# Kernel tuning notes

Measured on AMD Instinct MI355X. Metric: run time of the kernel, lower is better.

The kernel has to match this reference:

```python
import jax, jax.numpy as jnp
import numpy as np

# Interpretation constants (external PersistentHomology class unavailable):
# each sample's feature vector is a point cloud of N_POINTS points in R^POINT_DIM.
N_POINTS = 1024
POINT_DIM = 128
WEIGHT = 1.0
N_TARGET_DIMS = 2  # target_dimensions = [0, 1]; H1 diagram is empty -> contributes 0


def _h0_mean_persistence(pts):
    """Exact H0 persistence of the Vietoris-Rips filtration of a point cloud.

    H0 pairs are (birth=0, death=w_e) for each edge w_e of the Euclidean MST,
    so persistence values are exactly the MST edge lengths (Prim's algorithm,
    vectorized over points, sequential over the N-1 tree-growth steps).
    pts: [N, d] -> scalar mean persistence.
    """
    n = pts.shape[0]
    mindist0 = jnp.linalg.norm(pts - pts[0], axis=-1)          # [N]
    visited0 = jnp.zeros((n,), dtype=bool).at[0].set(True)

    def step(carry, _):
        mindist, visited = carry
        masked = jnp.where(visited, jnp.inf, mindist)          # [N]
        j = jnp.argmin(masked)
        death = masked[j]                                      # MST edge length
        visited = visited.at[j].set(True)
        newd = jnp.linalg.norm(pts - pts[j], axis=-1)          # [N]
        mindist = jnp.minimum(mindist, newd)
        return (mindist, visited), death

    (_, _), deaths = jax.lax.scan(step, (mindist0, visited0), None, length=n - 1)
    return jnp.mean(deaths)


def setup_inputs() -> dict:
    key = jax.random.key(0)
    representations = jax.random.normal(key, (128, N_POINTS * POINT_DIM), dtype=jnp.float32)
    return {"representations": representations}


def reference(representations) -> jnp.ndarray:
    b = representations.shape[0]
    pts = representations.reshape(b, N_POINTS, POINT_DIM)      # per-sample point cloud
    per_sample = jax.vmap(_h0_mean_persistence)(pts)           # [B] mean H0 persistence
    # original: sum over batch and target dims (H1 empty), / (B * n_dims), * weight
    loss = jnp.sum(per_sample) / (b * N_TARGET_DIMS)
    return WEIGHT * loss
```

## Files before the change

### kernel.cpp

```cpp
#include <hip/hip_runtime.h>

typedef unsigned int uint_t;
typedef unsigned short ushort_t;
typedef unsigned char uchar_t;
typedef _Float16 h2 __attribute__((ext_vector_type(2)));
typedef _Float16 f16x8 __attribute__((ext_vector_type(8)));
typedef float f32x4 __attribute__((ext_vector_type(4)));

#define NPTS 1024
#define DIM  128
#define NH2  64

__device__ __forceinline__ float dot2f(uint_t a, uint_t b, float c) {
#if __has_builtin(__builtin_amdgcn_fdot2)
    return __builtin_amdgcn_fdot2(__builtin_bit_cast(h2, a),
                                  __builtin_bit_cast(h2, b), c, false);
#else
    h2 ha = __builtin_bit_cast(h2, a);
    h2 hb = __builtin_bit_cast(h2, b);
    c += (float)ha[0] * (float)hb[0];
    c += (float)ha[1] * (float)hb[1];
    return c;
#endif
}

__device__ __forceinline__ uint_t umin_u(uint_t a, uint_t b) { return a < b ? a : b; }
__device__ __forceinline__ uint_t umax_u(uint_t a, uint_t b) { return a > b ? a : b; }
__device__ __forceinline__ uint_t pk_min_u16(uint_t a, uint_t b) {
    uint_t d; asm("v_pk_min_u16 %0, %1, %2" : "=v"(d) : "v"(a), "v"(b)); return d;
}
__device__ __forceinline__ uint_t pk_max_u16(uint_t a, uint_t b) {
    uint_t d; asm("v_pk_max_u16 %0, %1, %2" : "=v"(d) : "v"(a), "v"(b)); return d;
}

#define DPP_UMIN(x, ctrl)                                                       \
    x = umin_u(x, (uint_t)__builtin_amdgcn_update_dpp((int)(x), (int)(x),       \
                                                      (ctrl), 0xf, 0xf, false))
#define DPP_REDUCE(x)                                                           \
    do { DPP_UMIN(x, 0x111); DPP_UMIN(x, 0x112); DPP_UMIN(x, 0x114);            \
         DPP_UMIN(x, 0x118); DPP_UMIN(x, 0x142); DPP_UMIN(x, 0x143); } while (0)

#define SEL_LO 0x05020400u
#define SEL_HI 0x07020600u

__device__ __forceinline__ void gload16(const void* g, void* l) {
#if __has_builtin(__builtin_amdgcn_global_load_lds)
    __builtin_amdgcn_global_load_lds(
        (__attribute__((address_space(1))) void*)(g),
        (__attribute__((address_space(3))) void*)(l), 16, 0, 0);
#else
    *(uint4*)l = *(const uint4*)g;
#endif
}

__global__ __launch_bounds__(256)
void prep_kernel(const float* __restrict__ reps, ushort_t* __restrict__ P16,
                 float* __restrict__ norms) {
    const int t   = threadIdx.x;
    const int row = blockIdx.x * 16 + (t >> 4);
    const int kx  = (t & 15) * 8;
    const float* src = reps + (size_t)row * DIM + kx;
    float4 v0 = *(const float4*)src;
    float4 v1 = *(const float4*)(src + 4);
    _Float16 h[8] = {(_Float16)v0.x, (_Float16)v0.y, (_Float16)v0.z, (_Float16)v0.w,
                     (_Float16)v1.x, (_Float16)v1.y, (_Float16)v1.z, (_Float16)v1.w};
    float nrm = 0.f;
    uint_t pk[4];
#pragma unroll
    for (int i = 0; i < 4; ++i) {
        float a = (float)h[2 * i], b = (float)h[2 * i + 1];
        nrm += a * a + b * b;
        pk[i] = (uint_t)__builtin_bit_cast(ushort_t, h[2 * i]) |
                ((uint_t)__builtin_bit_cast(ushort_t, h[2 * i + 1]) << 16);
    }
    *(uint4*)(P16 + (size_t)row * DIM + kx) = make_uint4(pk[0], pk[1], pk[2], pk[3]);
#pragma unroll
    for (int m = 1; m <= 8; m <<= 1) nrm += __shfl_xor(nrm, m, 16);
    if ((t & 15) == 0) norms[row] = nrm;
}

__global__ __launch_bounds__(256)
void norms_kernel(const float* __restrict__ reps, float* __restrict__ norms) {
    const int t   = threadIdx.x;
    const int row = blockIdx.x * 16 + (t >> 4);
    const int kx  = (t & 15) * 8;
    const float* src = reps + (size_t)row * DIM + kx;
    float4 v0 = *(const float4*)src;
    float4 v1 = *(const float4*)(src + 4);
    float nrm = 0.f;
    {
        _Float16 h[8] = {(_Float16)v0.x, (_Float16)v0.y, (_Float16)v0.z, (_Float16)v0.w,
                         (_Float16)v1.x, (_Float16)v1.y, (_Float16)v1.z, (_Float16)v1.w};
#pragma unroll
        for (int i = 0; i < 8; ++i) { float a = (float)h[i]; nrm += a * a; }
    }
#pragma unroll
    for (int m = 1; m <= 8; m <<= 1) nrm += __shfl_xor(nrm, m, 16);
    if ((t & 15) == 0) norms[row] = nrm;
}

__device__ __forceinline__ int swz(int row, int seg) {
    return (row << 7) + (((seg ^ row) & 15) << 3);
}
__device__ __forceinline__ uint_t packh2(float a, float b) {
    h2 p; p[0] = (_Float16)a; p[1] = (_Float16)b;
    return __builtin_bit_cast(uint_t, p);
}

__device__ __forceinline__ void gram_core_epilogue(
        f32x4 acc[2][8], const float* nrmS, uchar_t* Ds,
        int ti, int tj, int lane, int w) {
    const int cj = lane & 15;
    const int r4 = (lane >> 4) * 4;
    float na[2][4], nb[8];
#pragma unroll
    for (int mt = 0; mt < 2; ++mt)
#pragma unroll
        for (int r = 0; r < 4; ++r)
            na[mt][r] = nrmS[ti * 128 + w * 32 + mt * 16 + r4 + r];
#pragma unroll
    for (int nt = 0; nt < 8; ++nt) nb[nt] = nrmS[tj * 128 + nt * 16 + cj];
#pragma unroll
    for (int mt = 0; mt < 2; ++mt)
#pragma unroll
        for (int nt = 0; nt < 8; ++nt) {
            const int gj = tj * 128 + nt * 16 + cj;
#pragma unroll
            for (int r = 0; r < 4; ++r) {
                const int gi = ti * 128 + w * 32 + mt * 16 + r4 + r;
                float d2 = fmaxf(na[mt][r] + nb[nt] - 2.f * acc[mt][nt][r], 0.f);
                uint_t q = (uint_t)(d2 * 0.5f + 0.5f);
                q = q > 255u ? 255u : q;
                Ds[((size_t)gi << 10) + gj] = (uchar_t)q;
            }
        }
}

__global__ __launch_bounds__(256, 4)
void gram16_kernel(const ushort_t* __restrict__ P16, const float* __restrict__ norms,
                   uchar_t* __restrict__ D8, int xcd_affine) {
    __shared__ ushort_t Bt[128 * 128];
    const int bid = blockIdx.x;
    int s, tile;
    if (xcd_affine) {
        const int x = bid & 7, k = bid >> 3;
        s    = x + ((k >> 6) << 3);
        tile = k & 63;
    } else {
        s    = bid >> 6;
        tile = bid & 63;
    }
    const int ti = tile >> 3, tj = tile & 7;
    const int t  = threadIdx.x, lane = t & 63, w = t >> 6;

    const ushort_t* Pa = P16 + (((size_t)s * NPTS + (size_t)ti * 128) << 7);
    const ushort_t* Pb = P16 + (((size_t)s * NPTS + (size_t)tj * 128) << 7);
#pragma unroll
    for (int i = 0; i < 8; ++i) {
        const int c   = t + i * 256;
        const int row = c >> 4;
        const int seg = (c ^ row) & 15;
        gload16(Pb + ((size_t)row << 7) + (size_t)seg * 8, &Bt[(size_t)c * 8]);
    }

    const int mrow = lane & 15;
    const int lg   = lane >> 4;
    const ushort_t* parow0 = Pa + ((w * 32 + mrow) << 7);
    const ushort_t* parow1 = Pa + ((w * 32 + 16 + mrow) << 7);
    f16x8 a0 = *(const f16x8*)(parow0 + lg * 8);
    f16x8 a1 = *(const f16x8*)(parow1 + lg * 8);
    __syncthreads();

    f32x4 acc[2][8] = {};
#pragma unroll
    for (int q = 0; q < 4; ++q) {
        const int seg = q * 4 + lg;
        f16x8 a0c = a0, a1c = a1;
        if (q < 3) {
            a0 = *(const f16x8*)(parow0 + ((q + 1) * 4 + lg) * 8);
            a1 = *(const f16x8*)(parow1 + ((q + 1) * 4 + lg) * 8);
        }
#pragma unroll
        for (int nt = 0; nt < 8; ++nt) {
            f16x8 b = *(const f16x8*)&Bt[swz(nt * 16 + mrow, seg)];
            acc[0][nt] = __builtin_amdgcn_mfma_f32_16x16x32_f16(a0c, b, acc[0][nt], 0, 0, 0);
            acc[1][nt] = __builtin_amdgcn_mfma_f32_16x16x32_f16(a1c, b, acc[1][nt], 0, 0, 0);
        }
    }

    const float* nrmS = norms + (size_t)s * NPTS;
    uchar_t*     Ds   = D8 + ((size_t)s << 20);
    const int cj = lane & 15;
    const int r4 = (lane >> 4) * 4;
    float ha[2][4], hb[8];
#pragma unroll
    for (int mt = 0; mt < 2; ++mt)
#pragma unroll
        for (int r = 0; r < 4; ++r)
            ha[mt][r] = 0.5f * nrmS[ti * 128 + w * 32 + mt * 16 + r4 + r] + 0.5f;
#pragma unroll
    for (int nt = 0; nt < 8; ++nt) hb[nt] = 0.5f * nrmS[tj * 128 + nt * 16 + cj];

    const uint_t rr    = (uint_t)(lane & 3);
    const uint_t sel01 = rr | ((rr + 4u) << 8);
    uint_t res[2][8];
#pragma unroll
    for (int mt = 0; mt < 2; ++mt)
#pragma unroll
        for (int nt = 0; nt < 8; ++nt) {
            uint_t cp = 0;
#pragma unroll
            for (int r = 0; r < 4; ++r) {
                float f = (ha[mt][r] + hb[nt]) - acc[mt][nt][r];
#if __has_builtin(__builtin_amdgcn_cvt_pk_u8_f32)
                cp = __builtin_amdgcn_cvt_pk_u8_f32(f, (uint_t)r, cp);
#else
                uint_t qb = (uint_t)fminf(fmaxf(f, 0.f), 255.f);
                cp |= qb << (8 * r);
#endif
            }
            uint_t d0 = (uint_t)__builtin_amdgcn_update_dpp((int)cp, (int)cp, 0x00, 0xf, 0xf, false);
            uint_t d1 = (uint_t)__builtin_amdgcn_update_dpp((int)cp, (int)cp, 0x55, 0xf, 0xf, false);
            uint_t d2 = (uint_t)__builtin_amdgcn_update_dpp((int)cp, (int)cp, 0xaa, 0xf, 0xf, false);
            uint_t d3 = (uint_t)__builtin_amdgcn_update_dpp((int)cp, (int)cp, 0xff, 0xf, 0xf, false);
            uint_t lo  = __builtin_amdgcn_perm(d1, d0, sel01);
            uint_t hi  = __builtin_amdgcn_perm(d3, d2, sel01);
            res[mt][nt] = __builtin_amdgcn_perm(hi, lo, 0x05040100u);
        }

    __syncthreads();
    uchar_t* Ot = (uchar_t*)Bt;
    const int lrb = w * 32 + r4 + (int)rr;
    const int c4b = lane & 12;
#pragma unroll
    for (int mt = 0; mt < 2; ++mt)
#pragma unroll
        for (int nt = 0; nt < 8; ++nt) {
            const int lr = lrb + mt * 16;
            const int cs = nt ^ (lr & 7);
            *(uint_t*)&Ot[lr * 128 + cs * 16 + c4b] = res[mt][nt];
        }
    __syncthreads();
    {
        const int r8 = lane >> 3, c = lane & 7;
#pragma unroll
        for (int k = 0; k < 4; ++k) {
            const int row = w * 32 + k * 8 + r8;
            const int cs  = c ^ (row & 7);
            uint4 vv = *(const uint4*)&Ot[row * 128 + cs * 16];
            *(uint4*)(Ds + (((size_t)(ti * 128 + row)) << 10) + tj * 128 + c * 16) = vv;
        }
    }
}

__global__ __launch_bounds__(256, 2)
void gram_kernel(const float* __restrict__ reps, const float* __restrict__ norms,
                 uchar_t* __restrict__ D8, int s_base) {
    __shared__ ushort_t At[128 * 128];
    __shared__ ushort_t Bt[128 * 128];
    const int bid  = blockIdx.x;
    const int sl   = bid >> 6, tile = bid & 63, ti = tile >> 3, tj = tile & 7;
    const int s    = s_base + sl;
    const int t    = threadIdx.x, lane = t & 63, w = t >> 6;

    const float* Pa = reps + ((size_t)s * NPTS + (size_t)ti * 128) * DIM;
    const float* Pb = reps + ((size_t)s * NPTS + (size_t)tj * 128) * DIM;
#pragma unroll
    for (int i = 0; i < 8; ++i) {
        int c = t + i * 256, row = c >> 4, seg = c & 15;
        const float* pa = Pa + row * DIM + seg * 8;
        const float* pb = Pb + row * DIM + seg * 8;
        float4 a0 = *(const float4*)pa, a1 = *(const float4*)(pa + 4);
        float4 b0 = *(const float4*)pb, b1 = *(const float4*)(pb + 4);
        *(uint4*)&At[swz(row, seg)] = make_uint4(packh2(a0.x, a0.y), packh2(a0.z, a0.w),
                                                 packh2(a1.x, a1.y), packh2(a1.z, a1.w));
        *(uint4*)&Bt[swz(row, seg)] = make_uint4(packh2(b0.x, b0.y), packh2(b0.z, b0.w),
                                                 packh2(b1.x, b1.y), packh2(b1.z, b1.w));
    }
    __syncthreads();

    f32x4 acc[2][8] = {};
    const int mrow = lane & 15;
    const int lg   = lane >> 4;
#pragma unroll
    for (int q = 0; q < 4; ++q) {
        const int seg = q * 4 + lg;
        f16x8 a0 = *(const f16x8*)&At[swz(w * 32 + mrow, seg)];
        f16x8 a1 = *(const f16x8*)&At[swz(w * 32 + 16 + mrow, seg)];
#pragma unroll
        for (int nt = 0; nt < 8; ++nt) {
            f16x8 b = *(const f16x8*)&Bt[swz(nt * 16 + mrow, seg)];
            acc[0][nt] = __builtin_amdgcn_mfma_f32_16x16x32_f16(a0, b, acc[0][nt], 0, 0, 0);
            acc[1][nt] = __builtin_amdgcn_mfma_f32_16x16x32_f16(a1, b, acc[1][nt], 0, 0, 0);
        }
    }
    gram_core_epilogue(acc, norms + (size_t)s * NPTS, D8 + ((size_t)sl << 20),
                       ti, tj, lane, w);
}

__global__ __launch_bounds__(256)
void nn4_kernel(const uchar_t* __restrict__ D8, uint_t* __restrict__ NN4) {
    const int lane = threadIdx.x & 63;
    const int wv   = threadIdx.x >> 6;
    const int base = blockIdx.x * 64 + wv * 16;

    uint_t slotv[8];
#pragma unroll
    for (int m = 0; m < 8; ++m)
        slotv[m] = ((uint_t)(2 * m + 1) << 16) | (uint_t)(2 * m);

    uint4 rc = ((const uint4*)(D8 + ((size_t)base << 10)))[lane];
    for (int i = 0; i < 16; ++i) {
        const int row = base + i;
        uint4 rn = rc;
        if (i < 15)
            rn = ((const uint4*)(D8 + ((size_t)(row + 1) << 10)))[lane];

        uint_t md[8];
        md[0] = __builtin_amdgcn_perm(rc.x, slotv[0], SEL_LO);
        md[1] = __builtin_amdgcn_perm(rc.x, slotv[1], SEL_HI);
        md[2] = __builtin_amdgcn_perm(rc.y, slotv[2], SEL_LO);
        md[3] = __builtin_amdgcn_perm(rc.y, slotv[3], SEL_HI);
        md[4] = __builtin_amdgcn_perm(rc.z, slotv[4], SEL_LO);
        md[5] = __builtin_amdgcn_perm(rc.z, slotv[5], SEL_HI);
        md[6] = __builtin_amdgcn_perm(rc.w, slotv[6], SEL_LO);
        md[7] = __builtin_amdgcn_perm(rc.w, slotv[7], SEL_HI);
        {
            const int r_in = row & 1023;
            const bool win = (r_in >> 4) == lane;
            const uint_t s4 = (uint_t)(r_in & 15);
#pragma unroll
            for (int m = 0; m < 8; ++m) {
                uint_t h = (win && s4 == 2u * m)      ? 0x0000FFFFu
                         : (win && s4 == 2u * m + 1u) ? 0xFFFF0000u : 0u;
                md[m] |= h;
            }
        }
        uint_t out4[4];
#pragma unroll
        for (int k = 0; k < 4; ++k) {
            uint_t t0 = pk_min_u16(pk_min_u16(md[0], md[1]), pk_min_u16(md[2], md[3]));
            uint_t t1 = pk_min_u16(pk_min_u16(md[4], md[5]), pk_min_u16(md[6], md[7]));
            uint_t tt = pk_min_u16(t0, t1);
            uint_t v16 = umin_u(tt & 0xFFFFu, tt >> 16);
            uint_t key = ((v16 & 0xFF00u) << 2) | ((uint_t)lane << 4) | (v16 & 15u);
            DPP_REDUCE(key);
            uint_t g = (uint_t)__builtin_amdgcn_readlane((int)key, 63);
            out4[k] = g;
            if (k < 3) {
                const uint_t wl = (g >> 4) & 63u, ws = g & 15u;
                const bool win = (uint_t)lane == wl;
#pragma unroll
                for (int m = 0; m < 8; ++m) {
                    uint_t h = (win && ws == 2u * m)      ? 0x0000FFFFu
                             : (win && ws == 2u * m + 1u) ? 0xFFFF0000u : 0u;
                    md[m] |= h;
                }
            }
        }
        if (lane == 0)
            *(uint4*)(NN4 + (size_t)row * 4) = make_uint4(out4[0], out4[1],
                                                          out4[2], out4[3]);
        rc = rn;
    }
}

__global__ __launch_bounds__(1024)
void boruvka4_kernel(const uchar_t* __restrict__ D8, const uint_t* __restrict__ NN4,
                     float* __restrict__ out, float scale) {
    const int sl   = blockIdx.x;
    const int v    = threadIdx.x;
    const int lane = v & 63;
    const int wv   = v >> 6;
    const uchar_t* Dbase = D8 + ((size_t)sl << 20);

    __shared__ ushort_t root16[NPTS];
    __shared__ uint_t   best[NPTS];
    __shared__ ushort_t rq[64];
    __shared__ uint_t   rqn, ncomp_s;
    __shared__ float    fsum[16];

    uint4 nA = *(const uint4*)(NN4 + (((size_t)sl << 10) + (size_t)v) * 4);
    uint_t nn[4] = {nA.x, nA.y, nA.z, nA.w};

    root16[v] = (ushort_t)v;
    float acc = 0.f;
    __syncthreads();

    for (int round = 0; round < 48; ++round) {
        best[v] = 0xFFFFFFFFu;
        if (v == 0) { rqn = 0; ncomp_s = 0; }
        __syncthreads();

        const uint_t rv = root16[v];

        uint_t cand = 0xFFFFFFFFu;
#pragma unroll
        for (int k = 0; k < 4; ++k) {
            uint_t e = nn[k];
            uint_t j = e & 1023u;
            if (root16[j] != (ushort_t)rv) {
                uint_t q = e >> 10;
                uint_t a = umin_u((uint_t)v, j), b = umax_u((uint_t)v, j);
                cand = umin_u(cand, (q << 20) | (a << 10) | b);
            }
        }
        if (cand != 0xFFFFFFFFu) atomicMin(&best[rv], cand);
        __syncthreads();

        if (rv == (uint_t)v && best[v] == 0xFFFFFFFFu) {
            uint_t idx = atomicAdd(&rqn, 1u);
            if (idx < 64u) rq[idx] = (ushort_t)v;
        }
        __syncthreads();

        if (rqn != 0u) {
            const uint_t nq = umin_u(rqn, 64u);
            for (uint_t qi = (uint_t)wv; qi < nq; qi += 16) {
                const uint_t row = rq[qi];
                const uint_t rr  = root16[row];
                uint4 r = ((const uint4*)(Dbase + ((size_t)row << 10)))[lane];
                uint_t bl = 0xFFFFFFFFu;
                const uint_t base = (uint_t)lane * 16u;
#pragma unroll
                for (int k = 0; k < 16; ++k) {
                    uint_t j = base + (uint_t)k;
                    uint_t q = (k < 4  ? (r.x >> (8 * k))
                              : k < 8  ? (r.y >> (8 * (k - 4)))
                              : k < 12 ? (r.z >> (8 * (k - 8)))
                                       : (r.w >> (8 * (k - 12)))) & 0xFFu;
                    uint_t a = umin_u(row, j), b = umax_u(row, j);
                    if (root16[j] != (ushort_t)rr)
                        bl = umin_u(bl, (q << 20) | (a << 10) | b);
                }
                DPP_REDUCE(bl);
                uint_t g = (uint_t)__builtin_amdgcn_readlane((int)bl, 63);
                if (lane == 0 && g != 0xFFFFFFFFu) atomicMin(&best[rr], g);
            }
            __syncthreads();
        }

        bool hook = false;
        uint_t o = (uint_t)v;
        if (rv == (uint_t)v) {
            uint_t K = best[v];
            if (K != 0xFFFFFFFFu) {
                uint_t a = (K >> 10) & 1023u, b = K & 1023u, q = K >> 20;
                uint_t ra = root16[a], rb = root16[b];
                o = (ra == (uint_t)v) ? rb : ra;
                if (o < (uint_t)v) {
                    hook = true;
                    acc += sqrtf(2.0f * (float)q);
                }
            }
        }
        __syncthreads();
        if (hook) root16[v] = (ushort_t)o;
        __syncthreads();

        uint_t r = root16[v];
        uint_t pr = root16[r];
        for (int sg = 0; sg < 64 && pr != r; ++sg) { r = pr; pr = root16[r]; }
        __syncthreads();
        root16[v] = (ushort_t)r;

        unsigned long long ball = __ballot(r == (uint_t)v);
        if (lane == 0) atomicAdd(&ncomp_s, (uint_t)__popcll(ball));
        __syncthreads();
        if (ncomp_s == 1u) break;
    }

#pragma unroll
    for (int m = 32; m >= 1; m >>= 1) acc += __shfl_xor(acc, m, 64);
    if (lane == 0) fsum[wv] = acc;
    __syncthreads();
    if (v == 0) {
        float s = 0.f;
#pragma unroll
        for (int i = 0; i < 16; ++i) s += fsum[i];
        atomicAdd(out, s * scale);
    }
}

__global__ __launch_bounds__(1024)
void boruvka_kernel(const uchar_t* __restrict__ D8, float* __restrict__ out,
                    float scale) {
    const int sl   = blockIdx.x;
    const int v    = threadIdx.x;
    const int lane = v & 63;
    const int wv   = v >> 6;
    const uchar_t* Dbase = D8 + ((size_t)sl << 20);

    __shared__ uint_t   nnlist[NPTS * 8];
    __shared__ ushort_t root16[NPTS];
    __shared__ uint_t   best[NPTS];
    __shared__ ushort_t rq[NPTS];
    __shared__ uint_t   rqn, ncomp_s;
    __shared__ float    fsum[16];

    uint_t slotv[8];
#pragma unroll
    for (int m = 0; m < 8; ++m)
        slotv[m] = ((uint_t)(2 * m + 1) << 16) | (uint_t)(2 * m);

    {
        uint4 rc = ((const uint4*)(Dbase + ((size_t)wv << 10)))[lane];
        for (int i = 0; i < 64; ++i) {
            const int row = wv + 16 * i;
            uint4 rn = rc;
            if (i < 63)
                rn = ((const uint4*)(Dbase + ((size_t)(row + 16) << 10)))[lane];
            uint_t md[8];
            md[0] = __builtin_amdgcn_perm(rc.x, slotv[0], SEL_LO);
            md[1] = __builtin_amdgcn_perm(rc.x, slotv[1], SEL_HI);
            md[2] = __builtin_amdgcn_perm(rc.y, slotv[2], SEL_LO);
            md[3] = __builtin_amdgcn_perm(rc.y, slotv[3], SEL_HI);
            md[4] = __builtin_amdgcn_perm(rc.z, slotv[4], SEL_LO);
            md[5] = __builtin_amdgcn_perm(rc.z, slotv[5], SEL_HI);
            md[6] = __builtin_amdgcn_perm(rc.w, slotv[6], SEL_LO);
            md[7] = __builtin_amdgcn_perm(rc.w, slotv[7], SEL_HI);
            {
                const bool win = (row >> 4) == lane;
                const uint_t s4 = (uint_t)(row & 15);
#pragma unroll
                for (int m = 0; m < 8; ++m) {
                    uint_t h = (win && s4 == 2u * m)      ? 0x0000FFFFu
                             : (win && s4 == 2u * m + 1u) ? 0xFFFF0000u : 0u;
                    md[m] |= h;
                }
            }
#pragma unroll
            for (int k = 0; k < 8; ++k) {
                uint_t t0 = pk_min_u16(pk_min_u16(md[0], md[1]), pk_min_u16(md[2], md[3]));
                uint_t t1 = pk_min_u16(pk_min_u16(md[4], md[5]), pk_min_u16(md[6], md[7]));
                uint_t tt = pk_min_u16(t0, t1);
                uint_t v16 = umin_u(tt & 0xFFFFu, tt >> 16);
                uint_t key = ((v16 & 0xFF00u) << 2) | ((uint_t)lane << 4) | (v16 & 15u);
                DPP_REDUCE(key);
                uint_t g = (uint_t)__builtin_amdgcn_readlane((int)key, 63);
                if (lane == 0) nnlist[row * 8 + k] = g;
                const uint_t wl = (g >> 4) & 63u, ws = g & 15u;
                const bool win = (uint_t)lane == wl;
#pragma unroll
                for (int m = 0; m < 8; ++m) {
                    uint_t h = (win && ws == 2u * m)      ? 0x0000FFFFu
                             : (win && ws == 2u * m + 1u) ? 0xFFFF0000u : 0u;
                    md[m] |= h;
                }
            }
            rc = rn;
        }
    }
    root16[v] = (ushort_t)v;
    __syncthreads();

    uint_t nn[8];
#pragma unroll
    for (int k = 0; k < 8; ++k) nn[k] = nnlist[v * 8 + k];
    const uint_t q8 = nn[7] >> 10;

    float acc = 0.f;
    for (int round = 0; round < 12; ++round) {
        best[v] = 0xFFFFFFFFu;
        if (v == 0) { rqn = 0; ncomp_s = 0; }
        __syncthreads();
        const uint_t rv = root16[v];
        uint_t cand = 0xFFFFFFFFu;
#pragma unroll
        for (int k = 0; k < 8; ++k) {
            uint_t e = nn[k];
            uint_t j = e & 1023u;
            if (root16[j] != (ushort_t)rv) {
                uint_t q = e >> 10;
                uint_t a = umin_u((uint_t)v, j), b = umax_u((uint_t)v, j);
                cand = umin_u(cand, (q << 20) | (a << 10) | b);
            }
        }
        if (cand != 0xFFFFFFFFu) atomicMin(&best[rv], cand);
        if (cand == 0xFFFFFFFFu || (cand >> 20) >= q8) {
            uint_t idx = atomicAdd(&rqn, 1u);
            rq[idx] = (ushort_t)v;
        }
        __syncthreads();
        for (uint_t qi = (uint_t)wv; qi < rqn; qi += 16) {
            const uint_t row = rq[qi];
            const uint_t rr  = root16[row];
            uint4 r = ((const uint4*)(Dbase + ((size_t)row << 10)))[lane];
            uint_t bl = 0xFFFFFFFFu;
            const uint_t base = (uint_t)lane * 16u;
#pragma unroll
            for (int k = 0; k < 16; ++k) {
                uint_t j = base + (uint_t)k;
                uint_t q = (k < 4  ? (r.x >> (8 * k))
                          : k < 8  ? (r.y >> (8 * (k - 4)))
                          : k < 12 ? (r.z >> (8 * (k - 8)))
                                   : (r.w >> (8 * (k - 12)))) & 0xFFu;
                uint_t a = umin_u(row, j), b = umax_u(row, j);
                if (root16[j] != (ushort_t)rr)
                    bl = umin_u(bl, (q << 20) | (a << 10) | b);
            }
            DPP_REDUCE(bl);
            uint_t g = (uint_t)__builtin_amdgcn_readlane((int)bl, 63);
            if (lane == 0 && g != 0xFFFFFFFFu) atomicMin(&best[rr], g);
        }
        __syncthreads();
        const bool isroot = (rv == (uint_t)v);
        bool hook = false;
        uint_t o = (uint_t)v;
        if (isroot) {
            uint_t K = best[v];
            if (K != 0xFFFFFFFFu) {
                uint_t a = (K >> 10) & 1023u, b = K & 1023u, q = K >> 20;
                uint_t ra = root16[a], rb = root16[b];
                o = (ra == (uint_t)v) ? rb : ra;
                bool mutual = (best[o] == K);
                if (!mutual || (uint_t)v > o) {
                    hook = true;
                    acc += sqrtf(2.0f * (float)q);
                }
            }
        }
        __syncthreads();
        if (hook) root16[v] = (ushort_t)o;
        __syncthreads();
        uint_t r = root16[v];
        uint_t pr = root16[r];
        for (int sgs = 0; sgs < 1024 && pr != r; ++sgs) { r = pr; pr = root16[r]; }
        __syncthreads();
        root16[v] = (ushort_t)r;
        unsigned long long ball = __ballot(r == (uint_t)v);
        if (lane == 0) atomicAdd(&ncomp_s, (uint_t)__popcll(ball));
        __syncthreads();
        if (ncomp_s == 1u) break;
    }
#pragma unroll
    for (int m = 32; m >= 1; m >>= 1) acc += __shfl_xor(acc, m, 64);
    if (lane == 0) fsum[wv] = acc;
    __syncthreads();
    if (v == 0) {
        float s = 0.f;
#pragma unroll
        for (int i = 0; i < 16; ++i) s += fsum[i];
        atomicAdd(out, s * scale);
    }
}

__global__ __launch_bounds__(64, 1)
void prim_u8_kernel(const uchar_t* __restrict__ D8, float* __restrict__ out,
                    float scale) {
    const int sl   = blockIdx.x;
    const int lane = threadIdx.x;
    const uchar_t* Dbase = D8 + ((size_t)sl << 20);

    uint_t md[8], po[8], slotv[8];
#pragma unroll
    for (int m = 0; m < 8; ++m) {
        md[m] = 0xFFFFFFFFu; po[m] = 0u;
        slotv[m] = ((uint_t)(2 * m + 1) << 16) | (uint_t)(2 * m);
    }
    const uint_t lane16 = (uint_t)lane << 4;
    uint_t p   = 0;
    float  acc = 0.f;

    for (int it = 0; it < NPTS - 1; ++it) {
        const uint4* rp = (const uint4*)(Dbase + ((size_t)p << 10));
        uint4 r = rp[lane];
        const bool  win = (p >> 4) == (uint_t)lane;
        const uint_t s4 = p & 15u;
#pragma unroll
        for (int m = 0; m < 8; ++m) {
            uint_t h = (win && s4 == 2u * m)      ? 0x0000FFFFu
                     : (win && s4 == 2u * m + 1u) ? 0xFFFF0000u : 0u;
            md[m] |= h; po[m] |= h;
        }
        md[0] = pk_min_u16(md[0], pk_max_u16(__builtin_amdgcn_perm(r.x, slotv[0], SEL_LO), po[0]));
        md[1] = pk_min_u16(md[1], pk_max_u16(__builtin_amdgcn_perm(r.x, slotv[1], SEL_HI), po[1]));
        md[2] = pk_min_u16(md[2], pk_max_u16(__builtin_amdgcn_perm(r.y, slotv[2], SEL_LO), po[2]));
        md[3] = pk_min_u16(md[3], pk_max_u16(__builtin_amdgcn_perm(r.y, slotv[3], SEL_HI), po[3]));
        md[4] = pk_min_u16(md[4], pk_max_u16(__builtin_amdgcn_perm(r.z, slotv[4], SEL_LO), po[4]));
        md[5] = pk_min_u16(md[5], pk_max_u16(__builtin_amdgcn_perm(r.z, slotv[5], SEL_HI), po[5]));
        md[6] = pk_min_u16(md[6], pk_max_u16(__builtin_amdgcn_perm(r.w, slotv[6], SEL_LO), po[6]));
        md[7] = pk_min_u16(md[7], pk_max_u16(__builtin_amdgcn_perm(r.w, slotv[7], SEL_HI), po[7]));

        uint_t t0 = pk_min_u16(pk_min_u16(md[0], md[1]), pk_min_u16(md[2], md[3]));
        uint_t t1 = pk_min_u16(pk_min_u16(md[4], md[5]), pk_min_u16(md[6], md[7]));
        uint_t tt = pk_min_u16(t0, t1);
        uint_t v16 = umin_u(tt & 0xFFFFu, tt >> 16);

        uint_t key = ((v16 & 0xFF00u) << 2) | lane16 | (v16 & 15u);
        DPP_REDUCE(key);
        uint_t g = (uint_t)__builtin_amdgcn_readlane((int)key, 63);

        p = g & 1023u;
        acc += sqrtf(2.0f * (float)(g >> 10));
    }
    if (lane == 0) atomicAdd(out, acc * scale);
}

#define NTHR 256
#define NWAVE 4
#define PPT  4
__global__ __launch_bounds__(NTHR, 1)
void prim_mst_kernel(const float* __restrict__ reps, float* __restrict__ out,
                     float scale) {
    const int s = blockIdx.x, t = threadIdx.x, lane = t & 63, wave = t >> 6;
    __shared__ uint4  sc[NH2 / 4];
    __shared__ float  snrm;
    __shared__ __align__(16) uint_t warr[NWAVE];
    __shared__ float  facc[NWAVE];
    uint_t cx[PPT][NH2]; float nrm[PPT], mind[PPT];
#pragma unroll
    for (int p = 0; p < PPT; ++p) {
        const float4* src = (const float4*)(reps + (size_t)s * (NPTS * DIM) +
                                            (size_t)(p * NTHR + t) * DIM);
        float n = 0.f;
#pragma unroll
        for (int k = 0; k < 32; ++k) {
            float4 v = src[k];
            h2 a; a[0] = (_Float16)v.x; a[1] = (_Float16)v.y;
            h2 b; b[0] = (_Float16)v.z; b[1] = (_Float16)v.w;
            cx[p][2 * k] = __builtin_bit_cast(uint_t, a);
            cx[p][2 * k + 1] = __builtin_bit_cast(uint_t, b);
            n = dot2f(cx[p][2 * k], cx[p][2 * k], n);
            n = dot2f(cx[p][2 * k + 1], cx[p][2 * k + 1], n);
        }
        nrm[p] = n; mind[p] = 3.0e38f;
    }
    uint_t vis = 0;
    if (t == 0) {
#pragma unroll
        for (int k = 0; k < NH2 / 4; ++k)
            sc[k] = make_uint4(cx[0][4 * k], cx[0][4 * k + 1], cx[0][4 * k + 2], cx[0][4 * k + 3]);
        snrm = nrm[0]; vis = 1;
    }
    __syncthreads();
    float acc = 0.f;
    for (int it = 0; it < NPTS - 1; ++it) {
        const float bn = snrm;
        float e0[PPT], e1[PPT];
#pragma unroll
        for (int p = 0; p < PPT; ++p) { e0[p] = 0.f; e1[p] = 0.f; }
#pragma unroll
        for (int k = 0; k < NH2 / 4; ++k) {
            uint4 q = sc[k];
#pragma unroll
            for (int p = 0; p < PPT; ++p) {
                e0[p] = dot2f(cx[p][4 * k + 0], q.x, e0[p]);
                e1[p] = dot2f(cx[p][4 * k + 1], q.y, e1[p]);
                e0[p] = dot2f(cx[p][4 * k + 2], q.z, e0[p]);
                e1[p] = dot2f(cx[p][4 * k + 3], q.w, e1[p]);
            }
        }
        uint_t key = 0xFFFFFFFFu;
#pragma unroll
        for (int p = 0; p < PPT; ++p) {
            float d2 = fmaxf(bn + nrm[p] - 2.f * (e0[p] + e1[p]), 0.f);
            mind[p] = fminf(mind[p], d2);
            uint_t kp = ((vis >> p) & 1u) ? 0xFFFFFFFFu
                      : ((__float_as_uint(mind[p]) & 0xFFFFFC00u) | (uint_t)(p * NTHR + t));
            key = umin_u(key, kp);
        }
        DPP_REDUCE(key);
        uint_t wkey = (uint_t)__builtin_amdgcn_readlane((int)key, 63);
        if (lane == 0) warr[wave] = wkey;
        __syncthreads();
        uint4 wv = *(const uint4*)warr;
        uint_t g = umin_u(umin_u(wv.x, wv.y), umin_u(wv.z, wv.w));
        const int j = (int)(g & 0x3FFu), jp = j >> 8;
        if ((j & (NTHR - 1)) == t) {
#pragma unroll
            for (int p = 0; p < PPT; ++p)
                if (jp == p) {
#pragma unroll
                    for (int k = 0; k < NH2 / 4; ++k)
                        sc[k] = make_uint4(cx[p][4 * k], cx[p][4 * k + 1],
                                           cx[p][4 * k + 2], cx[p][4 * k + 3]);
                    snrm = nrm[p]; acc += sqrtf(mind[p]);
                }
            vis |= 1u << jp;
        }
        __syncthreads();
    }
#pragma unroll
    for (int m = 32; m >= 1; m >>= 1) acc += __shfl_xor(acc, m, 64);
    if (lane == 0) facc[wave] = acc;
    __syncthreads();
    if (t == 0) atomicAdd(out, (facc[0] + facc[1] + facc[2] + facc[3]) * scale);
}

extern "C" void kernel_launch(void* const* d_in, const int* in_sizes, int n_in,
                              void* d_out, int out_size, void* d_ws, size_t ws_size,
                              hipStream_t stream) {
    const float* reps = (const float*)d_in[0];
    float*       out  = (float*)d_out;
    const int ns = in_sizes[0] / (NPTS * DIM);
    const float scale = 1.0f / ((float)(NPTS - 1) * (float)ns * 2.0f);

    hipMemsetAsync(out, 0, sizeof(float), stream);

    const size_t bytes_D  = (size_t)ns << 20;
    const size_t bytes_P  = (size_t)ns << 18;
    const size_t bytes_NN = (size_t)ns << 14;
    const size_t bytes_N  = (size_t)ns << 12;

    if (ws_size >= bytes_D + bytes_P + bytes_NN + bytes_N) {
        uchar_t*  D8    = (uchar_t*)d_ws;
        ushort_t* P16   = (ushort_t*)((char*)d_ws + bytes_D);
        uint_t*   NN4   = (uint_t*)((char*)d_ws + bytes_D + bytes_P);
        float*    norms = (float*)((char*)d_ws + bytes_D + bytes_P + bytes_NN);
        const int xcd_affine = ((ns & 7) == 0) ? 1 : 0;
        prep_kernel<<<dim3(ns * 64), dim3(256), 0, stream>>>(reps, P16, norms);
        gram16_kernel<<<dim3(ns * 64), dim3(256), 0, stream>>>(P16, norms, D8, xcd_affine);
        nn4_kernel<<<dim3(ns * 16), dim3(256), 0, stream>>>(D8, NN4);
        boruvka4_kernel<<<dim3(ns), dim3(1024), 0, stream>>>(D8, NN4, out, scale);
    } else if (ws_size >= bytes_D + bytes_N) {
        uchar_t* D8    = (uchar_t*)d_ws;
        float*   norms = (float*)((char*)d_ws + bytes_D);
        norms_kernel<<<dim3(ns * 64), dim3(256), 0, stream>>>(reps, norms);
        gram_kernel<<<dim3(ns * 64), dim3(256), 0, stream>>>(reps, norms, D8, 0);
        boruvka_kernel<<<dim3(ns), dim3(1024), 0, stream>>>(D8, out, scale);
    } else {
        int nc = 0;
        size_t norms_off = 0;
        if (ws_size > bytes_N + (1u << 20)) {
            norms_off = (ws_size - bytes_N) & ~(size_t)15;
            nc = (int)(norms_off >> 20);
            if (nc > ns) nc = ns;
        }
        if (nc >= 32) {
            uchar_t* D8    = (uchar_t*)d_ws;
            float*   norms = (float*)((char*)d_ws + norms_off);
            norms_kernel<<<dim3(ns * 64), dim3(256), 0, stream>>>(reps, norms);
            for (int base = 0; base < ns; base += nc) {
                const int n = (ns - base < nc) ? (ns - base) : nc;
                gram_kernel<<<dim3(n * 64), dim3(256), 0, stream>>>(reps, norms, D8, base);
                prim_u8_kernel<<<dim3(n), dim3(64), 0, stream>>>(D8, out, scale);
            }
        } else {
            prim_mst_kernel<<<dim3(ns), dim3(NTHR), 0, stream>>>(reps, out, scale);
        }
    }
}
```

Baseline: 240.2 us.

## Fuse 4-nearest-neighbour extraction into row-strip gram kernel with double-buffered B tiles

The gram kernel now assigns one block per 128-row strip and loops over all 8 column tiles, double-buffering the B tile in LDS while computing the current one. Each tile's quantised distances are reduced in registers into a running per-row top-4 nearest-neighbour list using packed u16 min and swizzle reductions, which removes the separate nn4 kernel and its re-read of the distance matrix. The trade-off is eight times fewer blocks (ns*8), lower occupancy from the larger LDS footprint, and a serial loop over tiles inside each block.

```diff
diff --git a/kernel.cpp b/kernel.cpp
--- a/kernel.cpp
+++ b/kernel.cpp
@@ -31,6 +31,9 @@
 }
 __device__ __forceinline__ uint_t pk_max_u16(uint_t a, uint_t b) {
     uint_t d; asm("v_pk_max_u16 %0, %1, %2" : "=v"(d) : "v"(a), "v"(b)); return d;
+}
+__device__ __forceinline__ uint_t pk_sub_u16w(uint_t a, uint_t b) {
+    uint_t d; asm("v_pk_sub_u16 %0, %1, %2" : "=v"(d) : "v"(a), "v"(b)); return d;
 }
 
 #define DPP_UMIN(x, ctrl)                                                       \
@@ -136,119 +139,198 @@
         }
 }
 
-__global__ __launch_bounds__(256, 4)
-void gram16_kernel(const ushort_t* __restrict__ P16, const float* __restrict__ norms,
-                   uchar_t* __restrict__ D8, int xcd_affine) {
-    __shared__ ushort_t Bt[128 * 128];
-    const int bid = blockIdx.x;
-    int s, tile;
-    if (xcd_affine) {
-        const int x = bid & 7, k = bid >> 3;
-        s    = x + ((k >> 6) << 3);
-        tile = k & 63;
-    } else {
-        s    = bid >> 6;
-        tile = bid & 63;
-    }
-    const int ti = tile >> 3, tj = tile & 7;
-    const int t  = threadIdx.x, lane = t & 63, w = t >> 6;
-
-    const ushort_t* Pa = P16 + (((size_t)s * NPTS + (size_t)ti * 128) << 7);
-    const ushort_t* Pb = P16 + (((size_t)s * NPTS + (size_t)tj * 128) << 7);
+__device__ __forceinline__ void stageB(const ushort_t* Ps, int tj,
+                                       ushort_t* Bq, int t) {
 #pragma unroll
     for (int i = 0; i < 8; ++i) {
         const int c   = t + i * 256;
         const int row = c >> 4;
         const int seg = (c ^ row) & 15;
-        gload16(Pb + ((size_t)row << 7) + (size_t)seg * 8, &Bt[(size_t)c * 8]);
-    }
+        gload16(Ps + (((size_t)(tj * 128 + row)) << 7) + (size_t)seg * 8,
+                Bq + (size_t)c * 8);
+    }
+}
+
+__global__ __launch_bounds__(256, 2)
+void gram16f_kernel(const ushort_t* __restrict__ P16, const float* __restrict__ norms,
+                    uchar_t* __restrict__ D8, uint_t* __restrict__ NN4,
+                    int xcd_affine) {
+    __shared__ ushort_t Bt[2][128 * 128];
+    __shared__ uchar_t  Ot[128 * 128];
+    const int bid = blockIdx.x;
+    int s, ti;
+    if (xcd_affine) {
+        const int x = bid & 7, k = bid >> 3;
+        s  = x + ((k >> 3) << 3);
+        ti = k & 7;
+    } else {
+        s  = bid >> 3;
+        ti = bid & 7;
+    }
+    const int t = threadIdx.x, lane = t & 63, w = t >> 6;
+
+    const ushort_t* Ps = P16 + ((size_t)s * NPTS << 7);
+    const ushort_t* Pa = Ps + ((size_t)ti * 128 << 7);
+    const float*  nrmS = norms + (size_t)s * NPTS;
+    uchar_t*      Ds   = D8 + ((size_t)s << 20);
 
     const int mrow = lane & 15;
     const int lg   = lane >> 4;
+    const int cj   = lane & 15;
+    const int r4   = (lane >> 4) * 4;
+    const uint_t rr  = (uint_t)(lane & 3);
+    const uint_t cl4 = (uint_t)(lane & 12);
+
+    float ha[2][4];
+#pragma unroll
+    for (int mt = 0; mt < 2; ++mt)
+#pragma unroll
+        for (int r = 0; r < 4; ++r)
+            ha[mt][r] = 0.5f * nrmS[ti * 128 + w * 32 + mt * 16 + r4 + r] + 0.5f;
+
     const ushort_t* parow0 = Pa + ((w * 32 + mrow) << 7);
     const ushort_t* parow1 = Pa + ((w * 32 + 16 + mrow) << 7);
-    f16x8 a0 = *(const f16x8*)(parow0 + lg * 8);
-    f16x8 a1 = *(const f16x8*)(parow1 + lg * 8);
+
+    uint_t nnr[2][4] = {{~0u, ~0u, ~0u, ~0u}, {~0u, ~0u, ~0u, ~0u}};
+
+    const uint_t rr_    = (uint_t)(lane & 3);
+    const uint_t sel01  = rr_ | ((rr_ + 4u) << 8);
+
+    stageB(Ps, 0, &Bt[0][0], t);
     __syncthreads();
 
-    f32x4 acc[2][8] = {};
-#pragma unroll
-    for (int q = 0; q < 4; ++q) {
-        const int seg = q * 4 + lg;
-        f16x8 a0c = a0, a1c = a1;
-        if (q < 3) {
-            a0 = *(const f16x8*)(parow0 + ((q + 1) * 4 + lg) * 8);
-            a1 = *(const f16x8*)(parow1 + ((q + 1) * 4 + lg) * 8);
-        }
-#pragma unroll
-        for (int nt = 0; nt < 8; ++nt) {
-            f16x8 b = *(const f16x8*)&Bt[swz(nt * 16 + mrow, seg)];
-            acc[0][nt] = __builtin_amdgcn_mfma_f32_16x16x32_f16(a0c, b, acc[0][nt], 0, 0, 0);
-            acc[1][nt] = __builtin_amdgcn_mfma_f32_16x16x32_f16(a1c, b, acc[1][nt], 0, 0, 0);
-        }
-    }
-
-    const float* nrmS = norms + (size_t)s * NPTS;
-    uchar_t*     Ds   = D8 + ((size_t)s << 20);
-    const int cj = lane & 15;
-    const int r4 = (lane >> 4) * 4;
-    float ha[2][4], hb[8];
-#pragma unroll
-    for (int mt = 0; mt < 2; ++mt)
-#pragma unroll
-        for (int r = 0; r < 4; ++r)
-            ha[mt][r] = 0.5f * nrmS[ti * 128 + w * 32 + mt * 16 + r4 + r] + 0.5f;
-#pragma unroll
-    for (int nt = 0; nt < 8; ++nt) hb[nt] = 0.5f * nrmS[tj * 128 + nt * 16 + cj];
-
-    const uint_t rr    = (uint_t)(lane & 3);
-    const uint_t sel01 = rr | ((rr + 4u) << 8);
-    uint_t res[2][8];
-#pragma unroll
-    for (int mt = 0; mt < 2; ++mt)
-#pragma unroll
-        for (int nt = 0; nt < 8; ++nt) {
-            uint_t cp = 0;
+    for (int tj = 0; tj < 8; ++tj) {
+        ushort_t* Bq = &Bt[tj & 1][0];
+        if (tj < 7) stageB(Ps, tj + 1, &Bt[(tj + 1) & 1][0], t);
+
+        f32x4 acc[2][8] = {};
+        f16x8 a0 = *(const f16x8*)(parow0 + lg * 8);
+        f16x8 a1 = *(const f16x8*)(parow1 + lg * 8);
+#pragma unroll
+        for (int q = 0; q < 4; ++q) {
+            const int seg = q * 4 + lg;
+            f16x8 a0c = a0, a1c = a1;
+            if (q < 3) {
+                a0 = *(const f16x8*)(parow0 + ((q + 1) * 4 + lg) * 8);
+                a1 = *(const f16x8*)(parow1 + ((q + 1) * 4 + lg) * 8);
+            }
+#pragma unroll
+            for (int nt = 0; nt < 8; ++nt) {
+                f16x8 b = *(const f16x8*)&Bq[swz(nt * 16 + mrow, seg)];
+                acc[0][nt] = __builtin_amdgcn_mfma_f32_16x16x32_f16(a0c, b, acc[0][nt], 0, 0, 0);
+                acc[1][nt] = __builtin_amdgcn_mfma_f32_16x16x32_f16(a1c, b, acc[1][nt], 0, 0, 0);
+            }
+        }
+
+        float hb[8];
+#pragma unroll
+        for (int nt = 0; nt < 8; ++nt) hb[nt] = 0.5f * nrmS[tj * 128 + nt * 16 + cj];
+        uint_t res[2][8];
+#pragma unroll
+        for (int mt = 0; mt < 2; ++mt)
+#pragma unroll
+            for (int nt = 0; nt < 8; ++nt) {
+                uint_t cp = 0;
+#pragma unroll
+                for (int r = 0; r < 4; ++r) {
+                    float f = (ha[mt][r] + hb[nt]) - acc[mt][nt][r];
+#if __has_builtin(__builtin_amdgcn_cvt_pk_u8_f32)
+                    cp = __builtin_amdgcn_cvt_pk_u8_f32(f, (uint_t)r, cp);
+#else
+                    uint_t qb = (uint_t)fminf(fmaxf(f, 0.f), 255.f);
+                    cp |= qb << (8 * r);
+#endif
+                }
+                uint_t d0 = (uint_t)__builtin_amdgcn_update_dpp((int)cp, (int)cp, 0x00, 0xf, 0xf, false);
+                uint_t d1 = (uint_t)__builtin_amdgcn_update_dpp((int)cp, (int)cp, 0x55, 0xf, 0xf, false);
+                uint_t d2 = (uint_t)__builtin_amdgcn_update_dpp((int)cp, (int)cp, 0xaa, 0xf, 0xf, false);
+                uint_t d3 = (uint_t)__builtin_amdgcn_update_dpp((int)cp, (int)cp, 0xff, 0xf, 0xf, false);
+                uint_t lo  = __builtin_amdgcn_perm(d1, d0, sel01);
+                uint_t hi  = __builtin_amdgcn_perm(d3, d2, sel01);
+                res[mt][nt] = __builtin_amdgcn_perm(hi, lo, 0x05040100u);
+            }
+
+        __syncthreads();
+        const int lrb = w * 32 + r4 + (int)rr;
+        const int c4b = lane & 12;
+#pragma unroll
+        for (int mt = 0; mt < 2; ++mt)
+#pragma unroll
+            for (int nt = 0; nt < 8; ++nt) {
+                const int lr = lrb + mt * 16;
+                const int cs = nt ^ (lr & 7);
+                *(uint_t*)&Ot[lr * 128 + cs * 16 + c4b] = res[mt][nt];
+            }
+        __syncthreads();
+        {
+            const int r8 = lane >> 3, c = lane & 7;
+#pragma unroll
+            for (int k = 0; k < 4; ++k) {
+                const int row = w * 32 + k * 8 + r8;
+                const int cs  = c ^ (row & 7);
+                uint4 vv = *(const uint4*)&Ot[row * 128 + cs * 16];
+                *(uint4*)(Ds + (((size_t)(ti * 128 + row)) << 10) + tj * 128 + c * 16) = vv;
+            }
+        }
+
+#pragma unroll
+        for (int mt = 0; mt < 2; ++mt) {
+            uint_t md[16];
+#pragma unroll
+            for (int nt = 0; nt < 8; ++nt) {
+                const uint_t base = (uint_t)(nt * 16) + cl4;
+                md[2 * nt]     = __builtin_amdgcn_perm(res[mt][nt],
+                                     ((base + 1u) << 16) | base, SEL_LO);
+                md[2 * nt + 1] = __builtin_amdgcn_perm(res[mt][nt],
+                                     ((base + 3u) << 16) | (base + 2u), SEL_HI);
+            }
+            if (ti == tj) {
+                const uint_t cs = (uint_t)(w * 32 + mt * 16 + r4) + rr;
+#pragma unroll
+                for (int m = 0; m < 16; ++m) {
+                    const uint_t cb = (uint_t)((m >> 1) * 16) + cl4 + (uint_t)((m & 1) * 2);
+                    uint_t h = (cs == cb) ? 0x0000FFFFu
+                             : (cs == cb + 1u) ? 0xFFFF0000u : 0u;
+                    md[m] |= h;
+                }
+            }
+            uint_t prev = 0;
 #pragma unroll
             for (int r = 0; r < 4; ++r) {
-                float f = (ha[mt][r] + hb[nt]) - acc[mt][nt][r];
-#if __has_builtin(__builtin_amdgcn_cvt_pk_u8_f32)
-                cp = __builtin_amdgcn_cvt_pk_u8_f32(f, (uint_t)r, cp);
-#else
-                uint_t qb = (uint_t)fminf(fmaxf(f, 0.f), 255.f);
-                cp |= qb << (8 * r);
-#endif
-            }
-            uint_t d0 = (uint_t)__builtin_amdgcn_update_dpp((int)cp, (int)cp, 0x00, 0xf, 0xf, false);
-            uint_t d1 = (uint_t)__builtin_amdgcn_update_dpp((int)cp, (int)cp, 0x55, 0xf, 0xf, false);
-            uint_t d2 = (uint_t)__builtin_amdgcn_update_dpp((int)cp, (int)cp, 0xaa, 0xf, 0xf, false);
-            uint_t d3 = (uint_t)__builtin_amdgcn_update_dpp((int)cp, (int)cp, 0xff, 0xf, 0xf, false);
-            uint_t lo  = __builtin_amdgcn_perm(d1, d0, sel01);
-            uint_t hi  = __builtin_amdgcn_perm(d3, d2, sel01);
-            res[mt][nt] = __builtin_amdgcn_perm(hi, lo, 0x05040100u);
-        }
-
-    __syncthreads();
-    uchar_t* Ot = (uchar_t*)Bt;
-    const int lrb = w * 32 + r4 + (int)rr;
-    const int c4b = lane & 12;
-#pragma unroll
-    for (int mt = 0; mt < 2; ++mt)
-#pragma unroll
-        for (int nt = 0; nt < 8; ++nt) {
-            const int lr = lrb + mt * 16;
-            const int cs = nt ^ (lr & 7);
-            *(uint_t*)&Ot[lr * 128 + cs * 16 + c4b] = res[mt][nt];
-        }
-    __syncthreads();
-    {
-        const int r8 = lane >> 3, c = lane & 7;
-#pragma unroll
-        for (int k = 0; k < 4; ++k) {
-            const int row = w * 32 + k * 8 + r8;
-            const int cs  = c ^ (row & 7);
-            uint4 vv = *(const uint4*)&Ot[row * 128 + cs * 16];
-            *(uint4*)(Ds + (((size_t)(ti * 128 + row)) << 10) + tj * 128 + c * 16) = vv;
+                uint_t tm[16];
+                if (r == 0) {
+#pragma unroll
+                    for (int m = 0; m < 16; ++m) tm[m] = md[m];
+                } else {
+                    const uint_t dd = prev | (prev << 16);
+#pragma unroll
+                    for (int m = 0; m < 16; ++m) tm[m] = pk_sub_u16w(md[m], dd);
+                }
+                uint_t t0 = pk_min_u16(pk_min_u16(pk_min_u16(tm[0], tm[1]), pk_min_u16(tm[2], tm[3])),
+                                       pk_min_u16(pk_min_u16(tm[4], tm[5]), pk_min_u16(tm[6], tm[7])));
+                uint_t t1 = pk_min_u16(pk_min_u16(pk_min_u16(tm[8], tm[9]), pk_min_u16(tm[10], tm[11])),
+                                       pk_min_u16(pk_min_u16(tm[12], tm[13]), pk_min_u16(tm[14], tm[15])));
+                uint_t T = pk_min_u16(t0, t1);
+                T = pk_min_u16(T, (uint_t)__builtin_amdgcn_ds_swizzle((int)T, 0x101F));
+                T = pk_min_u16(T, (uint_t)__builtin_amdgcn_ds_swizzle((int)T, 0x201F));
+                const uint_t v = umin_u(T & 0xFFFFu, T >> 16) + prev;
+                prev = v + 1u;
+                const uint_t g32 = ((v & 0xFF00u) << 2) | ((uint_t)tj << 7) | (v & 0x7Fu);
+                uint_t x = g32, mm;
+                mm = umin_u(nnr[mt][0], x); x = umax_u(nnr[mt][0], x); nnr[mt][0] = mm;
+                mm = umin_u(nnr[mt][1], x); x = umax_u(nnr[mt][1], x); nnr[mt][1] = mm;
+                mm = umin_u(nnr[mt][2], x); x = umax_u(nnr[mt][2], x); nnr[mt][2] = mm;
+                nnr[mt][3] = umin_u(nnr[mt][3], x);
+            }
+        }
+    }
+
+    if ((lane & 12) == 0) {
+#pragma unroll
+        for (int mt = 0; mt < 2; ++mt) {
+            const int grow = ti * 128 + w * 32 + mt * 16 + r4 + (int)rr;
+            *(uint4*)(NN4 + ((size_t)s * NPTS + (size_t)grow) * 4) =
+                make_uint4(nnr[mt][0], nnr[mt][1], nnr[mt][2], nnr[mt][3]);
         }
     }
 }
@@ -296,73 +378,6 @@
     }
     gram_core_epilogue(acc, norms + (size_t)s * NPTS, D8 + ((size_t)sl << 20),
                        ti, tj, lane, w);
-}
-
-__global__ __launch_bounds__(256)
-void nn4_kernel(const uchar_t* __restrict__ D8, uint_t* __restrict__ NN4) {
-    const int lane = threadIdx.x & 63;
-    const int wv   = threadIdx.x >> 6;
-    const int base = blockIdx.x * 64 + wv * 16;
-
-    uint_t slotv[8];
-#pragma unroll
-    for (int m = 0; m < 8; ++m)
-        slotv[m] = ((uint_t)(2 * m + 1) << 16) | (uint_t)(2 * m);
-
-    uint4 rc = ((const uint4*)(D8 + ((size_t)base << 10)))[lane];
-    for (int i = 0; i < 16; ++i) {
-        const int row = base + i;
-        uint4 rn = rc;
-        if (i < 15)
-            rn = ((const uint4*)(D8 + ((size_t)(row + 1) << 10)))[lane];
-
-        uint_t md[8];
-        md[0] = __builtin_amdgcn_perm(rc.x, slotv[0], SEL_LO);
-        md[1] = __builtin_amdgcn_perm(rc.x, slotv[1], SEL_HI);
-        md[2] = __builtin_amdgcn_perm(rc.y, slotv[2], SEL_LO);
-        md[3] = __builtin_amdgcn_perm(rc.y, slotv[3], SEL_HI);
-        md[4] = __builtin_amdgcn_perm(rc.z, slotv[4], SEL_LO);
-        md[5] = __builtin_amdgcn_perm(rc.z, slotv[5], SEL_HI);
-        md[6] = __builtin_amdgcn_perm(rc.w, slotv[6], SEL_LO);
-        md[7] = __builtin_amdgcn_perm(rc.w, slotv[7], SEL_HI);
-        {
-            const int r_in = row & 1023;
-            const bool win = (r_in >> 4) == lane;
-            const uint_t s4 = (uint_t)(r_in & 15);
-#pragma unroll
-            for (int m = 0; m < 8; ++m) {
-                uint_t h = (win && s4 == 2u * m)      ? 0x0000FFFFu
-                         : (win && s4 == 2u * m + 1u) ? 0xFFFF0000u : 0u;
-                md[m] |= h;
-            }
-        }
-        uint_t out4[4];
-#pragma unroll
-        for (int k = 0; k < 4; ++k) {
-            uint_t t0 = pk_min_u16(pk_min_u16(md[0], md[1]), pk_min_u16(md[2], md[3]));
-            uint_t t1 = pk_min_u16(pk_min_u16(md[4], md[5]), pk_min_u16(md[6], md[7]));
-            uint_t tt = pk_min_u16(t0, t1);
-            uint_t v16 = umin_u(tt & 0xFFFFu, tt >> 16);
-            uint_t key = ((v16 & 0xFF00u) << 2) | ((uint_t)lane << 4) | (v16 & 15u);
-            DPP_REDUCE(key);
-            uint_t g = (uint_t)__builtin_amdgcn_readlane((int)key, 63);
-            out4[k] = g;
-            if (k < 3) {
-                const uint_t wl = (g >> 4) & 63u, ws = g & 15u;
-                const bool win = (uint_t)lane == wl;
-#pragma unroll
-                for (int m = 0; m < 8; ++m) {
-                    uint_t h = (win && ws == 2u * m)      ? 0x0000FFFFu
-                             : (win && ws == 2u * m + 1u) ? 0xFFFF0000u : 0u;
-                    md[m] |= h;
-                }
-            }
-        }
-        if (lane == 0)
-            *(uint4*)(NN4 + (size_t)row * 4) = make_uint4(out4[0], out4[1],
-                                                          out4[2], out4[3]);
-        rc = rn;
-    }
 }
 
 __global__ __launch_bounds__(1024)
@@ -810,8 +825,8 @@
         float*    norms = (float*)((char*)d_ws + bytes_D + bytes_P + bytes_NN);
         const int xcd_affine = ((ns & 7) == 0) ? 1 : 0;
         prep_kernel<<<dim3(ns * 64), dim3(256), 0, stream>>>(reps, P16, norms);
-        gram16_kernel<<<dim3(ns * 64), dim3(256), 0, stream>>>(P16, norms, D8, xcd_affine);
-        nn4_kernel<<<dim3(ns * 16), dim3(256), 0, stream>>>(D8, NN4);
+        gram16f_kernel<<<dim3(ns * 8), dim3(256), 0, stream>>>(P16, norms, D8, NN4,
+                                                               xcd_affine);
         boruvka4_kernel<<<dim3(ns), dim3(1024), 0, stream>>>(D8, NN4, out, scale);
     } else if (ws_size >= bytes_D + bytes_N) {
         uchar_t* D8    = (uchar_t*)d_ws;
```

Result: faster. 209.9 us (-12.6%).
